# Optimization experiments

Measured on AMD Instinct MI355X. Metric: run time of the kernel, lower is better.

Reference implementation:

```python
import jax, jax.numpy as jnp
import numpy as np

EPS = 1e-12  # matches torch F.normalize eps


def _l2norm(t):
    n = jnp.linalg.norm(t, axis=-1, keepdims=True)
    return t / jnp.maximum(n, EPS)


def setup_inputs() -> dict:
    key = jax.random.key(0)
    ks = jax.random.split(key, 10)
    B, N, C = 2, 2048, 384
    nH, hd = 12, 32
    inp = {
        "x": jax.random.normal(ks[0], (B, N, C), jnp.float32),
        "q_w": jax.random.normal(ks[1], (C, C), jnp.float32) * 0.02,
        "q_b": jax.random.normal(ks[2], (C,), jnp.float32) * 0.02,
        "kv_w": jax.random.normal(ks[3], (2 * C, C), jnp.float32) * 0.02,
        "kv_b": jax.random.normal(ks[4], (2 * C,), jnp.float32) * 0.02,
        "query_embedding": jax.random.normal(ks[5], (nH, 1, hd), jnp.float32) * 0.02,
        # init of temperature in torch: log(exp(1/0.24) - 1)
        "temperature": jnp.full((nH, 1, 1), float(np.log(np.exp(1.0 / 0.24) - 1.0)), jnp.float32),
        "pos_bias": jax.random.normal(ks[7], (nH, N), jnp.float32) * 0.0004,
        "proj_w": jax.random.normal(ks[8], (C, C), jnp.float32) * 0.02,
        "proj_b": jax.random.normal(ks[9], (C,), jnp.float32) * 0.02,
        "D": 8, "H": 16, "W": 16,
    }
    return inp


def reference(x, q_w, q_b, kv_w, kv_b, query_embedding, temperature, pos_bias, proj_w, proj_b, D, H, W):
    B, N, C = x.shape
    nH, hd = query_embedding.shape[0], query_embedding.shape[2]
    assert N == D * H * W
    # q projection -> [B, nH, N, hd], cosine-normalized
    q = (x @ q_w.T + q_b).reshape(B, N, nH, hd).transpose(0, 2, 1, 3)
    q = _l2norm(q)
    # additive query embedding, softplus temperature, seq-length (log N) scale
    scale = jax.nn.softplus(temperature) * jnp.float32(np.log(N))  # [nH,1,1]
    q = (q + query_embedding[None]) * scale[None]
    # kv projection
    kv = x @ kv_w.T + kv_b  # [B, N, 2C]
    k, v = kv[..., :C], kv[..., C:]
    k = _l2norm(k.reshape(B, N, nH, hd).transpose(0, 2, 1, 3))
    v = v.reshape(B, N, nH, hd).transpose(0, 2, 1, 3)
    # scores with per-head learned positional bias over keys
    attn = jnp.einsum("bhqd,bhkd->bhqk", q, k) + pos_bias[None, :, None, :]
    attn = jax.nn.softmax(attn, axis=-1)
    out = jnp.einsum("bhqk,bhkd->bhqd", attn, v)
    out = out.transpose(0, 2, 1, 3).reshape(B, N, C)
    return out @ proj_w.T + proj_b
```

## Files before the change

### kernel.cpp

```cpp
#include <hip/hip_runtime.h>

#define LOG2E 1.4426950408889634f

typedef __bf16 bf16x8 __attribute__((ext_vector_type(8)));
typedef short s16x4 __attribute__((ext_vector_type(4)));
typedef float f32x4 __attribute__((ext_vector_type(4)));

#define BB 2
#define NN 2048
#define CC 384
#define NH 12
#define HD 32
#define MROWS (BB * NN)

__device__ __forceinline__ unsigned short f2bf(float f) {
  __bf16 h = (__bf16)f;
  return __builtin_bit_cast(unsigned short, h);
}

__device__ __forceinline__ bf16x8 ldg_bf8(const unsigned short* p) {
  uint4 v = *reinterpret_cast<const uint4*>(p);
  return __builtin_bit_cast(bf16x8, v);
}

__device__ __forceinline__ float fexp2(float x) {
#if __has_builtin(__builtin_amdgcn_exp2f)
  return __builtin_amdgcn_exp2f(x);
#else
  return exp2f(x);
#endif
}

__device__ __forceinline__ s16x4 pack_bf4(float a, float b, float c, float d) {
#if __has_builtin(__builtin_amdgcn_cvt_pk_bf16_f32)
  auto lo = __builtin_amdgcn_cvt_pk_bf16_f32(a, b);
  auto hi = __builtin_amdgcn_cvt_pk_bf16_f32(c, d);
  uint2 u = {__builtin_bit_cast(unsigned int, lo),
             __builtin_bit_cast(unsigned int, hi)};
  return __builtin_bit_cast(s16x4, u);
#else
  s16x4 r = {(short)f2bf(a), (short)f2bf(b), (short)f2bf(c), (short)f2bf(d)};
  return r;
#endif
}

typedef __attribute__((address_space(1))) const void gas_void;
typedef __attribute__((address_space(3))) void las_void;
__device__ __forceinline__ void gload_lds16(const void* g, void* l) {
  __builtin_amdgcn_global_load_lds((gas_void*)(unsigned long long)g,
                                   (las_void*)(unsigned long long)l, 16, 0, 0);
}

__device__ __forceinline__ f32x4 mfma32(bf16x8 a, bf16x8 b, f32x4 c) {
  return __builtin_amdgcn_mfma_f32_16x16x32_bf16(a, b, c, 0, 0, 0);
}

__device__ __forceinline__ f32x4 mfma16(s16x4 a, s16x4 b, f32x4 c) {
#if defined(__HIP_DEVICE_COMPILE__)
#if __has_builtin(__builtin_amdgcn_mfma_f32_16x16x16bf16_1k)
  return __builtin_amdgcn_mfma_f32_16x16x16bf16_1k(a, b, c, 0, 0, 0);
#else
  asm volatile("v_mfma_f32_16x16x16_bf16 %0, %1, %2, %0"
               : "+v"(c) : "v"(a), "v"(b));
  return c;
#endif
#else
  return c;
#endif
}

__global__ __launch_bounds__(256) void prep_kernel(
    const float* __restrict__ x, const float* __restrict__ q_w,
    const float* __restrict__ kv_w, const float* __restrict__ proj_w,
    const float* __restrict__ pos_bias, unsigned short* __restrict__ xb,
    unsigned short* __restrict__ qwb, unsigned short* __restrict__ kvwb,
    unsigned short* __restrict__ pwb, float* __restrict__ bias2) {
  int i = blockIdx.x * 256 + threadIdx.x;
  if (i < 1572864) { xb[i] = f2bf(x[i]); return; }
  i -= 1572864;
  if (i < 147456) { qwb[i] = f2bf(q_w[i]); return; }
  i -= 147456;
  if (i < 294912) { kvwb[i] = f2bf(kv_w[i]); return; }
  i -= 294912;
  if (i < 147456) { pwb[i] = f2bf(proj_w[i]); return; }
  i -= 147456;
  bias2[i] = pos_bias[i] * LOG2E;
}

__global__ __launch_bounds__(256, 4) void gemm_qkv_norm_kernel(
    const unsigned short* __restrict__ xb, const unsigned short* __restrict__ qwb,
    const unsigned short* __restrict__ kvwb, const float* __restrict__ q_b,
    const float* __restrict__ kv_b, const float* __restrict__ qe,
    const float* __restrict__ temperature, unsigned short* __restrict__ Qs,
    unsigned short* __restrict__ Kn, unsigned short* __restrict__ VT) {
  __shared__ alignas(16) char smem[2][20480];
  int wave = threadIdx.x >> 6, lane = threadIdx.x & 63;
  int c = lane & 15, quad = lane >> 4;
  int h = blockIdx.y;
  int m0b = blockIdx.x * 64;
  int cid = wave * 64 + lane;

  auto stage = [&](int buf, int kk) {
    char* base = smem[buf];
#pragma unroll
    for (int j = 0; j < 2; ++j) {
      int chunk = j * 256 + cid;
      int row = chunk >> 3, e = chunk & 7;
      gload_lds16(xb + (long)(m0b + row) * CC + kk + e * 8,
                  base + j * 4096 + wave * 1024);
    }
#pragma unroll
    for (int j = 0; j < 3; ++j) {
      int chunk = j * 256 + cid;
      int row = chunk >> 3, e = chunk & 7;
      const unsigned short* src;
      if (row < 32)      src = qwb + (long)(h * 32 + row) * CC;
      else if (row < 64) src = kvwb + (long)(h * 32 + (row - 32)) * CC;
      else               src = kvwb + (long)(CC + h * 32 + (row - 64)) * CC;
      gload_lds16(src + kk + e * 8, base + 8192 + j * 4096 + wave * 1024);
    }
  };

  f32x4 acc[6] = {};
  auto compute = [&](int buf) {
    const char* base = smem[buf];
#pragma unroll
    for (int kh = 0; kh < 2; ++kh) {
      bf16x8 a = *(const bf16x8*)(base + (wave * 16 + c) * 128 + kh * 64 + quad * 16);
#pragma unroll
      for (int t = 0; t < 6; ++t) {
        bf16x8 b = *(const bf16x8*)(base + 8192 + (t * 16 + c) * 128 + kh * 64 + quad * 16);
        acc[t] = mfma32(a, b, acc[t]);
      }
    }
  };

  stage(0, 0);
#pragma unroll 1
  for (int s = 0; s < 6; ++s) {
    __syncthreads();
    if (s < 5) stage((s + 1) & 1, (s + 1) * 64);
    compute(s & 1);
  }

  int m0 = m0b + wave * 16;
  float qb0 = q_b[h * 32 + c], qb1 = q_b[h * 32 + 16 + c];
  float kb0 = kv_b[h * 32 + c], kb1 = kv_b[h * 32 + 16 + c];
  float vb0 = kv_b[CC + h * 32 + c], vb1 = kv_b[CC + h * 32 + 16 + c];
  float qe0 = qe[h * HD + c], qe1 = qe[h * HD + 16 + c];
  float sc = log1pf(expf(temperature[h])) * 11.0f;
  int b = m0 >> 11;
  int nb = (m0 & 2047) + quad * 4;
  int pair = b * NH + h;
  unsigned short* qsb = Qs + ((long)pair * NN + nb) * HD;
  unsigned short* knb = Kn + ((long)pair * NN + nb) * HD;
  ushort4 vp0, vp1;
#pragma unroll
  for (int r = 0; r < 4; ++r) {
    float q0 = acc[0][r] + qb0, q1 = acc[1][r] + qb1;
    float k0 = acc[2][r] + kb0, k1 = acc[3][r] + kb1;
    float v0 = acc[4][r] + vb0, v1 = acc[5][r] + vb1;
    float qs = q0 * q0 + q1 * q1, ks = k0 * k0 + k1 * k1;
#pragma unroll
    for (int off = 8; off; off >>= 1) {
      qs += __shfl_xor(qs, off);
      ks += __shfl_xor(ks, off);
    }
    float qi = 1.0f / fmaxf(sqrtf(qs), 1e-12f);
    float ki = 1.0f / fmaxf(sqrtf(ks), 1e-12f);
    qsb[r * HD + c] = f2bf((q0 * qi + qe0) * sc);
    qsb[r * HD + 16 + c] = f2bf((q1 * qi + qe1) * sc);
    knb[r * HD + c] = f2bf(k0 * ki);
    knb[r * HD + 16 + c] = f2bf(k1 * ki);
    ((unsigned short*)&vp0)[r] = f2bf(v0);
    ((unsigned short*)&vp1)[r] = f2bf(v1);
  }
  *reinterpret_cast<ushort4*>(VT + ((long)pair * HD + c) * NN + nb) = vp0;
  *reinterpret_cast<ushort4*>(VT + ((long)pair * HD + 16 + c) * NN + nb) = vp1;
}

__global__ __launch_bounds__(256, 4) void attn_kernel(
    const unsigned short* __restrict__ Qs, const unsigned short* __restrict__ Kn,
    const unsigned short* __restrict__ VT, const float* __restrict__ bias2,
    unsigned short* __restrict__ ao) {
  __shared__ alignas(16) char smem[2][16384];
  __shared__ alignas(16) char biasl[8192];
  int wave = threadIdx.x >> 6, lane = threadIdx.x & 63;
  int c = lane & 15, quad = lane >> 4;
  int id = blockIdx.x;
  int xcd = id & 7, rr = id >> 3;
  int pair = (rr >> 5) * 8 + xcd;
  int qt = rr & 31;
  int h = pair % NH, b = pair / NH;
  const unsigned short* Qp = Qs + (long)pair * NN * HD;
  const char* Kg0 = (const char*)(Kn + (long)pair * NN * HD);
  const char* Vg0 = (const char*)(VT + (long)pair * HD * NN);
  const char* bp = (const char*)(bias2 + h * NN);
  int q0 = qt * 64 + wave * 16;
  bf16x8 qf = ldg_bf8(Qp + (long)(q0 + c) * HD + quad * 8);
  f32x4 o0 = {}, o1 = {};
  float rs = 0.f;

  const int koff = (c * 4 + quad) * 16;
  const int vchunk = wave * 64 + lane;

  auto stage = [&](int buf, int k0) {
    char* base = smem[buf];
    const char* Kg = Kg0 + (long)k0 * (HD * 2);
    const char* Vg = Vg0 + (long)k0 * 2;
#pragma unroll
    for (int j = 0; j < 2; ++j) {
      gload_lds16(Kg + (j * 4 + wave) * 1024 + koff,
                  base + j * 4096 + wave * 1024);
      int chunk = j * 256 + vchunk;
      int d = chunk >> 4, e = chunk & 15;
      int es = e ^ (d & 15);
      gload_lds16(Vg + (long)d * (NN * 2) + es * 16,
                  base + 8192 + j * 4096 + wave * 1024);
    }
  };

  auto compute = [&](int buf, int it) {
    const char* kb = smem[buf] + lane * 16;
    const char* vb = smem[buf] + 8192;
    const char* bl = biasl + it * 512 + quad * 16;
#pragma unroll
    for (int t8 = 0; t8 < 8; ++t8) {
      bf16x8 kf = *(const bf16x8*)(kb + t8 * 1024);
      f32x4 bbv = *(const f32x4*)(bl + t8 * 64);
      f32x4 s = mfma32(kf, qf, bbv);
      float p0 = fexp2(s[0]);
      float p1 = fexp2(s[1]);
      float p2 = fexp2(s[2]);
      float p3 = fexp2(s[3]);
      rs += (p0 + p1) + (p2 + p3);
      s16x4 pf = pack_bf4(p0, p1, p2, p3);
      int vsw = (((t8 * 2 + (quad >> 1)) ^ c) * 16) + (quad & 1) * 8;
      s16x4 vlo = *(const s16x4*)(vb + c * 256 + vsw);
      s16x4 vhi = *(const s16x4*)(vb + (c + 16) * 256 + vsw);
      o0 = mfma16(vlo, pf, o0);
      o1 = mfma16(vhi, pf, o1);
    }
  };

#pragma unroll
  for (int i = 0; i < 2; ++i)
    gload_lds16(bp + i * 4096 + wave * 1024 + lane * 16,
                biasl + i * 4096 + wave * 1024);
  stage(0, 0);
#pragma unroll 1
  for (int it = 0; it < 16; ++it) {
    __syncthreads();
    if (it < 15) stage((it + 1) & 1, (it + 1) * 128);
    compute(it & 1, it);
  }

  rs += __shfl_xor(rs, 16);
  rs += __shfl_xor(rs, 32);
  float inv = 1.0f / rs;
  unsigned short* op = ao + (long)(b * NN + q0 + c) * CC + h * HD + quad * 4;
  ushort4 s0, s1;
#pragma unroll
  for (int r = 0; r < 4; ++r) {
    ((unsigned short*)&s0)[r] = f2bf(o0[r] * inv);
    ((unsigned short*)&s1)[r] = f2bf(o1[r] * inv);
  }
  *reinterpret_cast<ushort4*>(op) = s0;
  *reinterpret_cast<ushort4*>(op + 16) = s1;
}

__global__ __launch_bounds__(256, 4) void proj_kernel(
    const unsigned short* __restrict__ ab, const unsigned short* __restrict__ pwb,
    const float* __restrict__ proj_b, float* __restrict__ out) {
  __shared__ alignas(16) char smem[2][16384];
  int wave = threadIdx.x >> 6, lane = threadIdx.x & 63;
  int c = lane & 15, quad = lane >> 4;
  int m0b = blockIdx.x * 64;
  int n0 = blockIdx.y * 64;
  int cid = wave * 64 + lane;

  auto stage = [&](int buf, int kk) {
    char* base = smem[buf];
#pragma unroll
    for (int j = 0; j < 2; ++j) {
      int chunk = j * 256 + cid;
      int row = chunk >> 3, e = chunk & 7;
      gload_lds16(ab + (long)(m0b + row) * CC + kk + e * 8,
                  base + j * 4096 + wave * 1024);
      gload_lds16(pwb + (long)(n0 + row) * CC + kk + e * 8,
                  base + 8192 + j * 4096 + wave * 1024);
    }
  };

  f32x4 acc[4] = {};
  auto compute = [&](int buf) {
    const char* base = smem[buf];
#pragma unroll
    for (int kh = 0; kh < 2; ++kh) {
      bf16x8 a = *(const bf16x8*)(base + (wave * 16 + c) * 128 + kh * 64 + quad * 16);
#pragma unroll
      for (int t = 0; t < 4; ++t) {
        bf16x8 b = *(const bf16x8*)(base + 8192 + (t * 16 + c) * 128 + kh * 64 + quad * 16);
        acc[t] = mfma32(a, b, acc[t]);
      }
    }
  };

  stage(0, 0);
#pragma unroll 1
  for (int s = 0; s < 6; ++s) {
    __syncthreads();
    if (s < 5) stage((s + 1) & 1, (s + 1) * 64);
    compute(s & 1);
  }

  int m0 = m0b + wave * 16;
#pragma unroll
  for (int t = 0; t < 4; ++t) {
    int o = n0 + t * 16 + c;
    float bv = proj_b[o];
#pragma unroll
    for (int r = 0; r < 4; ++r) {
      out[(long)(m0 + quad * 4 + r) * CC + o] = acc[t][r] + bv;
    }
  }
}

extern "C" void kernel_launch(void* const* d_in, const int* in_sizes, int n_in,
                              void* d_out, int out_size, void* d_ws, size_t ws_size,
                              hipStream_t stream) {
  const float* x = (const float*)d_in[0];
  const float* q_w = (const float*)d_in[1];
  const float* q_b = (const float*)d_in[2];
  const float* kv_w = (const float*)d_in[3];
  const float* kv_b = (const float*)d_in[4];
  const float* qe = (const float*)d_in[5];
  const float* temp = (const float*)d_in[6];
  const float* pos_bias = (const float*)d_in[7];
  const float* proj_w = (const float*)d_in[8];
  const float* proj_b = (const float*)d_in[9];
  float* out = (float*)d_out;

  char* ws = (char*)d_ws;
  unsigned short* xb = (unsigned short*)(ws + 0);
  unsigned short* qwb = (unsigned short*)(ws + 3145728);
  unsigned short* kvwb = (unsigned short*)(ws + 3440640);
  unsigned short* pwb = (unsigned short*)(ws + 4030464);
  unsigned short* Qs = (unsigned short*)(ws + 4325376);
  unsigned short* Kn = (unsigned short*)(ws + 7471104);
  unsigned short* VT = (unsigned short*)(ws + 10616832);
  unsigned short* ao = (unsigned short*)(ws + 13762560);
  float* bias2 = (float*)(ws + 16908288);

  prep_kernel<<<8544, 256, 0, stream>>>(x, q_w, kv_w, proj_w, pos_bias, xb, qwb,
                                        kvwb, pwb, bias2);
  gemm_qkv_norm_kernel<<<dim3(64, NH), 256, 0, stream>>>(xb, qwb, kvwb, q_b, kv_b,
                                                         qe, temp, Qs, Kn, VT);
  attn_kernel<<<768, 256, 0, stream>>>(Qs, Kn, VT, bias2, ao);
  proj_kernel<<<dim3(64, 6), 256, 0, stream>>>(ao, pwb, proj_b, out);
}
```

Baseline: 133.5 us.

## Split attention key range across two wave groups per block and combine

The attention block grows from 256 to 512 threads. The second group of four waves handles the second half of the keys (split-K) with its own double-buffered LDS tiles, so each group runs 8 iterations instead of 16. Partial outputs and row sums are merged through LDS at the end. This raises wave-level parallelism and shortens the serial loop, at the cost of more LDS per block (72KB), which may reduce how many blocks fit per CU, plus an extra combine step.

```diff
diff --git a/kernel.cpp b/kernel.cpp
--- a/kernel.cpp
+++ b/kernel.cpp
@@ -179,13 +179,14 @@
   *reinterpret_cast<ushort4*>(VT + ((long)pair * HD + 16 + c) * NN + nb) = vp1;
 }
 
-__global__ __launch_bounds__(256, 4) void attn_kernel(
+__global__ __launch_bounds__(512, 4) void attn_kernel(
     const unsigned short* __restrict__ Qs, const unsigned short* __restrict__ Kn,
     const unsigned short* __restrict__ VT, const float* __restrict__ bias2,
     unsigned short* __restrict__ ao) {
-  __shared__ alignas(16) char smem[2][16384];
+  __shared__ alignas(16) char smem[2][2][16384];
   __shared__ alignas(16) char biasl[8192];
   int wave = threadIdx.x >> 6, lane = threadIdx.x & 63;
+  int half = wave >> 2, sw = wave & 3;
   int c = lane & 15, quad = lane >> 4;
   int id = blockIdx.x;
   int xcd = id & 7, rr = id >> 3;
@@ -196,34 +197,33 @@
   const char* Kg0 = (const char*)(Kn + (long)pair * NN * HD);
   const char* Vg0 = (const char*)(VT + (long)pair * HD * NN);
   const char* bp = (const char*)(bias2 + h * NN);
-  int q0 = qt * 64 + wave * 16;
+  int q0 = qt * 64 + sw * 16;
   bf16x8 qf = ldg_bf8(Qp + (long)(q0 + c) * HD + quad * 8);
   f32x4 o0 = {}, o1 = {};
   float rs = 0.f;
 
   const int koff = (c * 4 + quad) * 16;
-  const int vchunk = wave * 64 + lane;
-
-  auto stage = [&](int buf, int k0) {
-    char* base = smem[buf];
-    const char* Kg = Kg0 + (long)k0 * (HD * 2);
-    const char* Vg = Vg0 + (long)k0 * 2;
+
+  auto stage = [&](int buf, int i) {
+    char* tb = smem[buf][half];
+    long krow0 = half * 1024 + i * 128;
+    const char* Kg = Kg0 + krow0 * (HD * 2);
+    const char* Vg = Vg0 + krow0 * 2;
 #pragma unroll
     for (int j = 0; j < 2; ++j) {
-      gload_lds16(Kg + (j * 4 + wave) * 1024 + koff,
-                  base + j * 4096 + wave * 1024);
-      int chunk = j * 256 + vchunk;
+      int ck = sw * 2 + j;
+      gload_lds16(Kg + ck * 1024 + koff, tb + ck * 1024);
+      int chunk = ck * 64 + lane;
       int d = chunk >> 4, e = chunk & 15;
       int es = e ^ (d & 15);
-      gload_lds16(Vg + (long)d * (NN * 2) + es * 16,
-                  base + 8192 + j * 4096 + wave * 1024);
-    }
-  };
-
-  auto compute = [&](int buf, int it) {
-    const char* kb = smem[buf] + lane * 16;
-    const char* vb = smem[buf] + 8192;
-    const char* bl = biasl + it * 512 + quad * 16;
+      gload_lds16(Vg + (long)d * (NN * 2) + es * 16, tb + 8192 + ck * 1024);
+    }
+  };
+
+  auto compute = [&](int buf, int i) {
+    const char* kb = smem[buf][half] + lane * 16;
+    const char* vb = smem[buf][half] + 8192;
+    const char* bl = biasl + (half * 8 + i) * 512 + quad * 16;
 #pragma unroll
     for (int t8 = 0; t8 < 8; ++t8) {
       bf16x8 kf = *(const bf16x8*)(kb + t8 * 1024);
@@ -243,30 +243,43 @@
     }
   };
 
-#pragma unroll
-  for (int i = 0; i < 2; ++i)
-    gload_lds16(bp + i * 4096 + wave * 1024 + lane * 16,
-                biasl + i * 4096 + wave * 1024);
+  gload_lds16(bp + wave * 1024 + lane * 16, biasl + wave * 1024);
   stage(0, 0);
 #pragma unroll 1
-  for (int it = 0; it < 16; ++it) {
+  for (int i = 0; i < 8; ++i) {
     __syncthreads();
-    if (it < 15) stage((it + 1) & 1, (it + 1) * 128);
-    compute(it & 1, it);
+    if (i < 7) stage((i + 1) & 1, i + 1);
+    compute(i & 1, i);
   }
 
   rs += __shfl_xor(rs, 16);
   rs += __shfl_xor(rs, 32);
-  float inv = 1.0f / rs;
-  unsigned short* op = ao + (long)(b * NN + q0 + c) * CC + h * HD + quad * 4;
-  ushort4 s0, s1;
-#pragma unroll
-  for (int r = 0; r < 4; ++r) {
-    ((unsigned short*)&s0)[r] = f2bf(o0[r] * inv);
-    ((unsigned short*)&s1)[r] = f2bf(o1[r] * inv);
-  }
-  *reinterpret_cast<ushort4*>(op) = s0;
-  *reinterpret_cast<ushort4*>(op + 16) = s1;
+
+  __syncthreads();
+  float* comb = (float*)&smem[0][0][0];
+  if (half == 1) {
+    float* p = comb + (sw * 64 + lane) * 9;
+#pragma unroll
+    for (int r = 0; r < 4; ++r) { p[r] = o0[r]; p[4 + r] = o1[r]; }
+    p[8] = rs;
+  }
+  __syncthreads();
+  if (half == 0) {
+    const float* p = comb + (sw * 64 + lane) * 9;
+#pragma unroll
+    for (int r = 0; r < 4; ++r) { o0[r] += p[r]; o1[r] += p[4 + r]; }
+    rs += p[8];
+    float inv = 1.0f / rs;
+    unsigned short* op = ao + (long)(b * NN + q0 + c) * CC + h * HD + quad * 4;
+    ushort4 s0, s1;
+#pragma unroll
+    for (int r = 0; r < 4; ++r) {
+      ((unsigned short*)&s0)[r] = f2bf(o0[r] * inv);
+      ((unsigned short*)&s1)[r] = f2bf(o1[r] * inv);
+    }
+    *reinterpret_cast<ushort4*>(op) = s0;
+    *reinterpret_cast<ushort4*>(op + 16) = s1;
+  }
 }
 
 __global__ __launch_bounds__(256, 4) void proj_kernel(
@@ -356,6 +369,6 @@
                                         kvwb, pwb, bias2);
   gemm_qkv_norm_kernel<<<dim3(64, NH), 256, 0, stream>>>(xb, qwb, kvwb, q_b, kv_b,
                                                          qe, temp, Qs, Kn, VT);
-  attn_kernel<<<768, 256, 0, stream>>>(Qs, Kn, VT, bias2, ao);
+  attn_kernel<<<768, 512, 0, stream>>>(Qs, Kn, VT, bias2, ao);
   proj_kernel<<<dim3(64, 6), 256, 0, stream>>>(ao, pwb, proj_b, out);
 }
```

New measurement: 132.9 us (median of 2 runs). Within noise of the previous version (-0.4%).

## Process two query tiles per wave in attention to reuse staged K/V

Applied to the files above, without the earlier changes.

Each wave now handles 32 query rows instead of 16, so every block covers 128 queries, and the grid is halved to 384 blocks. Each K fragment and V fragment loaded from LDS feeds two score MFMAs and four PV MFMAs, which halves global K/V staging traffic per query and the LDS reads per MFMA. The cost is more accumulator and exp registers per wave and fewer blocks, only 384 for 256 CUs, which may leave the device poorly balanced.

```diff
diff --git a/kernel.cpp b/kernel.cpp
--- a/kernel.cpp
+++ b/kernel.cpp
@@ -189,29 +189,30 @@
   int c = lane & 15, quad = lane >> 4;
   int id = blockIdx.x;
   int xcd = id & 7, rr = id >> 3;
-  int pair = (rr >> 5) * 8 + xcd;
-  int qt = rr & 31;
+  int pair = (rr >> 4) * 8 + xcd;
+  int qt = rr & 15;
   int h = pair % NH, b = pair / NH;
   const unsigned short* Qp = Qs + (long)pair * NN * HD;
   const char* Kg0 = (const char*)(Kn + (long)pair * NN * HD);
   const char* Vg0 = (const char*)(VT + (long)pair * HD * NN);
   const char* bp = (const char*)(bias2 + h * NN);
-  int q0 = qt * 64 + wave * 16;
-  bf16x8 qf = ldg_bf8(Qp + (long)(q0 + c) * HD + quad * 8);
-  f32x4 o0 = {}, o1 = {};
-  float rs = 0.f;
+  int q0 = qt * 128 + wave * 32;
+  bf16x8 qf0 = ldg_bf8(Qp + (long)(q0 + c) * HD + quad * 8);
+  bf16x8 qf1 = ldg_bf8(Qp + (long)(q0 + 16 + c) * HD + quad * 8);
+  f32x4 o0a = {}, o1a = {}, o0b = {}, o1b = {};
+  float rs0 = 0.f, rs1 = 0.f;
 
   const int koff = (c * 4 + quad) * 16;
   const int vchunk = wave * 64 + lane;
 
-  auto stage = [&](int buf, int k0) {
+  auto stage = [&](int buf, int i) {
     char* base = smem[buf];
-    const char* Kg = Kg0 + (long)k0 * (HD * 2);
-    const char* Vg = Vg0 + (long)k0 * 2;
+    const char* Kg = Kg0 + (long)i * 8192;
+    const char* Vg = Vg0 + (long)i * 256;
 #pragma unroll
     for (int j = 0; j < 2; ++j) {
       gload_lds16(Kg + (j * 4 + wave) * 1024 + koff,
-                  base + j * 4096 + wave * 1024);
+                  base + (j * 4 + wave) * 1024);
       int chunk = j * 256 + vchunk;
       int d = chunk >> 4, e = chunk & 15;
       int es = e ^ (d & 15);
@@ -228,18 +229,23 @@
     for (int t8 = 0; t8 < 8; ++t8) {
       bf16x8 kf = *(const bf16x8*)(kb + t8 * 1024);
       f32x4 bbv = *(const f32x4*)(bl + t8 * 64);
-      f32x4 s = mfma32(kf, qf, bbv);
-      float p0 = fexp2(s[0]);
-      float p1 = fexp2(s[1]);
-      float p2 = fexp2(s[2]);
-      float p3 = fexp2(s[3]);
-      rs += (p0 + p1) + (p2 + p3);
-      s16x4 pf = pack_bf4(p0, p1, p2, p3);
+      f32x4 sa = mfma32(kf, qf0, bbv);
+      f32x4 sb = mfma32(kf, qf1, bbv);
+      float pa0 = fexp2(sa[0]), pa1 = fexp2(sa[1]);
+      float pa2 = fexp2(sa[2]), pa3 = fexp2(sa[3]);
+      float pb0 = fexp2(sb[0]), pb1 = fexp2(sb[1]);
+      float pb2 = fexp2(sb[2]), pb3 = fexp2(sb[3]);
+      rs0 += (pa0 + pa1) + (pa2 + pa3);
+      rs1 += (pb0 + pb1) + (pb2 + pb3);
+      s16x4 pfa = pack_bf4(pa0, pa1, pa2, pa3);
+      s16x4 pfb = pack_bf4(pb0, pb1, pb2, pb3);
       int vsw = (((t8 * 2 + (quad >> 1)) ^ c) * 16) + (quad & 1) * 8;
       s16x4 vlo = *(const s16x4*)(vb + c * 256 + vsw);
       s16x4 vhi = *(const s16x4*)(vb + (c + 16) * 256 + vsw);
-      o0 = mfma16(vlo, pf, o0);
-      o1 = mfma16(vhi, pf, o1);
+      o0a = mfma16(vlo, pfa, o0a);
+      o1a = mfma16(vhi, pfa, o1a);
+      o0b = mfma16(vlo, pfb, o0b);
+      o1b = mfma16(vhi, pfb, o1b);
     }
   };
 
@@ -251,22 +257,29 @@
 #pragma unroll 1
   for (int it = 0; it < 16; ++it) {
     __syncthreads();
-    if (it < 15) stage((it + 1) & 1, (it + 1) * 128);
+    if (it < 15) stage((it + 1) & 1, it + 1);
     compute(it & 1, it);
   }
 
-  rs += __shfl_xor(rs, 16);
-  rs += __shfl_xor(rs, 32);
-  float inv = 1.0f / rs;
-  unsigned short* op = ao + (long)(b * NN + q0 + c) * CC + h * HD + quad * 4;
-  ushort4 s0, s1;
+  rs0 += __shfl_xor(rs0, 16);
+  rs0 += __shfl_xor(rs0, 32);
+  rs1 += __shfl_xor(rs1, 16);
+  rs1 += __shfl_xor(rs1, 32);
+  float inv0 = 1.0f / rs0, inv1 = 1.0f / rs1;
+  unsigned short* op0 = ao + (long)(b * NN + q0 + c) * CC + h * HD + quad * 4;
+  unsigned short* op1 = ao + (long)(b * NN + q0 + 16 + c) * CC + h * HD + quad * 4;
+  ushort4 s0, s1, s2, s3;
 #pragma unroll
   for (int r = 0; r < 4; ++r) {
-    ((unsigned short*)&s0)[r] = f2bf(o0[r] * inv);
-    ((unsigned short*)&s1)[r] = f2bf(o1[r] * inv);
-  }
-  *reinterpret_cast<ushort4*>(op) = s0;
-  *reinterpret_cast<ushort4*>(op + 16) = s1;
+    ((unsigned short*)&s0)[r] = f2bf(o0a[r] * inv0);
+    ((unsigned short*)&s1)[r] = f2bf(o1a[r] * inv0);
+    ((unsigned short*)&s2)[r] = f2bf(o0b[r] * inv1);
+    ((unsigned short*)&s3)[r] = f2bf(o1b[r] * inv1);
+  }
+  *reinterpret_cast<ushort4*>(op0) = s0;
+  *reinterpret_cast<ushort4*>(op0 + 16) = s1;
+  *reinterpret_cast<ushort4*>(op1) = s2;
+  *reinterpret_cast<ushort4*>(op1 + 16) = s3;
 }
 
 __global__ __launch_bounds__(256, 4) void proj_kernel(
@@ -356,6 +369,6 @@
                                         kvwb, pwb, bias2);
   gemm_qkv_norm_kernel<<<dim3(64, NH), 256, 0, stream>>>(xb, qwb, kvwb, q_b, kv_b,
                                                          qe, temp, Qs, Kn, VT);
-  attn_kernel<<<768, 256, 0, stream>>>(Qs, Kn, VT, bias2, ao);
+  attn_kernel<<<384, 256, 0, stream>>>(Qs, Kn, VT, bias2, ao);
   proj_kernel<<<dim3(64, 6), 256, 0, stream>>>(ao, pwb, proj_b, out);
 }
```

Result: slower. 141.8 us (+6.2%).
